# Kernel tuning notes

Measured on AMD Instinct MI355X. Metric: run time of the kernel, lower is better.

Reference implementation:

```python
import jax, jax.numpy as jnp
import numpy as np

B, T, D_IN = 32, 32, 128
N_SLOTS, M_LEN = 512, 64
NUM_SHIFT, NUM_READ, NUM_WRITE = 3, 4, 1
CTRL_DIM = 256
READ_HEAD_LEN = 3 + M_LEN + NUM_SHIFT            # k, beta, g, s, gamma
WRITE_HEAD_LEN = READ_HEAD_LEN + 2 * M_LEN       # + erase, add vectors
INSTR_DIM = NUM_READ * READ_HEAD_LEN + NUM_WRITE * WRITE_HEAD_LEN


def setup_inputs() -> dict:
    key = jax.random.key(0)
    ks = jax.random.split(key, 4)
    def glorot(k, shape):
        lim = np.sqrt(6.0 / (shape[0] + shape[1])).astype(np.float32)
        return jax.random.uniform(k, shape, jnp.float32, -lim, lim)
    return {
        "x": jax.random.normal(ks[0], (B, T, D_IN), jnp.float32),
        "Wc": glorot(ks[1], (D_IN + NUM_READ * M_LEN, CTRL_DIM)),
        "bc": jnp.zeros((CTRL_DIM,), jnp.float32),
        "heads_kernel": glorot(ks[2], (CTRL_DIM, INSTR_DIM)),
        "heads_bias": jnp.zeros((INSTR_DIM,), jnp.float32),
    }


def _parse_heads(h):
    # h: (B, H, 3 + M + S) -> k, beta, g, s, gamma per _get_weight_vector
    k = h[..., :M_LEN]
    b = jnp.exp(h[..., M_LEN])
    g = jax.nn.sigmoid(h[..., M_LEN + 1])
    s = jax.nn.softmax(h[..., M_LEN + 2:M_LEN + 2 + NUM_SHIFT], axis=-1)
    t = jax.nn.softplus(h[..., M_LEN + 2 + NUM_SHIFT]) + 1.0
    return k, b, g, s, t


def _address(Mem, w_prev, k, b, g, s, t):
    # Mem:(B,N,M) k:(B,H,M) w_prev:(B,H,N) b,g,t:(B,H) s:(B,H,S)
    eps = 1e-8
    Mn = jnp.linalg.norm(Mem, axis=-1)                       # (B,N)
    kn = jnp.linalg.norm(k, axis=-1)                         # (B,H)
    sim = jnp.einsum('bhm,bnm->bhn', k, Mem) / (kn[..., None] * Mn[:, None, :] + eps)
    wc = jax.nn.softmax(b[..., None] * sim, axis=-1)         # content
    wg = g[..., None] * wc + (1.0 - g[..., None]) * w_prev   # gate
    half = NUM_SHIFT // 2                                    # circular shift conv
    wsh = sum(s[..., i:i + 1] * jnp.roll(wg, i - half, axis=-1) for i in range(NUM_SHIFT))
    wt = wsh ** t[..., None]                                 # sharpen
    return wt / (jnp.sum(wt, axis=-1, keepdims=True) + eps)


def _ntm_forward(x, Wc, bc, heads_kernel, heads_bias):
    def step(carry, x_t):
        r, rw, ww, Mem = carry
        # dense controller on [x_t, old read vectors]
        ctrl_in = jnp.concatenate([x_t, r.reshape(B, -1)], axis=-1)
        h = jnp.tanh(ctrl_in @ Wc + bc)                      # controller_out == instr
        instr = h @ heads_kernel + heads_bias                # (B, INSTR_DIM)
        rh = instr[:, :NUM_READ * READ_HEAD_LEN].reshape(B, NUM_READ, READ_HEAD_LEN)
        wh = instr[:, NUM_READ * READ_HEAD_LEN:].reshape(B, NUM_WRITE, WRITE_HEAD_LEN)
        rw_n = _address(Mem, rw, *_parse_heads(rh))
        ww_n = _address(Mem, ww, *_parse_heads(wh[..., :READ_HEAD_LEN]))
        e = wh[..., READ_HEAD_LEN:READ_HEAD_LEN + M_LEN]     # raw erase (no sigmoid, as in source)
        a = wh[..., READ_HEAD_LEN + M_LEN:]                  # raw add
        # erase all heads, then add all heads (source loops erase first)
        Mem = Mem * jnp.prod(1.0 - ww_n[..., :, None] * e[..., None, :], axis=1)
        Mem = Mem + jnp.einsum('bwn,bwm->bnm', ww_n, a)
        r_n = jnp.einsum('bnm,brn->brm', Mem, rw_n)          # read
        return (r_n, rw_n, ww_n, Mem), h

    init = (jnp.zeros((B, NUM_READ, M_LEN), jnp.float32),
            jnp.zeros((B, NUM_READ, N_SLOTS), jnp.float32),
            jnp.zeros((B, NUM_WRITE, N_SLOTS), jnp.float32),
            jnp.zeros((B, N_SLOTS, M_LEN), jnp.float32))
    _, outs = jax.lax.scan(step, init, jnp.swapaxes(x, 0, 1))  # time-major
    return outs[-1]  # return_sequences=False -> last controller output (B, CTRL_DIM)


def reference(x, Wc, bc, heads_kernel, heads_bias):
    return _ntm_forward(x, Wc, bc, heads_kernel, heads_bias)
```

## Files before the change

### kernel.cpp

```cpp
#include <hip/hip_runtime.h>
#include <math.h>

#define BB 32
#define TT 32
#define D_INX 128
#define NSLOT 512
#define MLEN 64
#define NREAD 4
#define NHEAD 5
#define CDIM 256
#define IDIM 478
#define RHL 70
#define NT 512

#define XP_SZ   1048576
#define WCT_OFF XP_SZ
#define HKB_OFF (XP_SZ + 262144)

typedef short bf8 __attribute__((ext_vector_type(8)));
typedef float f32x4 __attribute__((ext_vector_type(4)));

struct SMem {
    float mem[NSLOT * MLEN];
    float w4[NSLOT * 4];
    float ww[NSLOT];
    float mn[NSLOT];
    float ctrl[256];
    float h[CDIM];
    float instr[480];
    float k[NHEAD * MLEN];
    float e[MLEN];
    float a[MLEN];
    float u[NHEAD * NSLOT];
};

__device__ __forceinline__ float rlane(float v, int l) {
    return __int_as_float(__builtin_amdgcn_readlane(__float_as_int(v), l));
}

__device__ __forceinline__ void cvt_hi_lo(const float* a, bf8* hi, bf8* lo) {
    union { unsigned u[4]; bf8 v; } H, L;
#pragma unroll
    for (int p = 0; p < 4; ++p) {
        unsigned hu;
        asm("v_cvt_pk_bf16_f32 %0, %1, %2" : "=v"(hu) : "v"(a[2 * p]), "v"(a[2 * p + 1]));
        H.u[p] = hu;
        float h0 = __uint_as_float(hu << 16);
        float h1 = __uint_as_float(hu & 0xffff0000u);
        float l0 = a[2 * p] - h0;
        float l1 = a[2 * p + 1] - h1;
        unsigned lu;
        asm("v_cvt_pk_bf16_f32 %0, %1, %2" : "=v"(lu) : "v"(l0), "v"(l1));
        L.u[p] = lu;
    }
    *hi = H.v; *lo = L.v;
}

__global__ void pack_kernel(const float* __restrict__ Wc, const float* __restrict__ Hk,
                            float* __restrict__ wct, float* __restrict__ hkb)
{
    int idx = blockIdx.x * 256 + threadIdx.x;
    if (idx < 256 * 256) {
        int i = idx >> 8, col = idx & 255;
        wct[((i >> 3) * 256 + col) * 8 + (i & 7)] = Wc[(128 + i) * 256 + col];
    }
    if (idx < 256 * 478) {
        int i = idx / 478, col = idx - i * 478;
        hkb[((i >> 3) * 478 + col) * 8 + (i & 7)] = Hk[i * 478 + col];
    }
}

__global__ __launch_bounds__(256)
void xpart_kernel(const float* __restrict__ x, const float* __restrict__ Wc,
                  const float* __restrict__ bc, float* __restrict__ xp)
{
    __shared__ float xs[D_INX];
    const int bt = blockIdx.x, col = threadIdx.x;
    if (col < D_INX) xs[col] = x[(size_t)bt * D_INX + col];
    __syncthreads();
    float acc = bc[col];
#pragma unroll 8
    for (int k = 0; k < D_INX; ++k) acc += xs[k] * Wc[k * 256 + col];
    xp[(size_t)bt * CDIM + col] = acc;
}

#define P1_CHUNK(cg_) do {                                                      \
    const float4 w0 = wqa[(cg_) * 512];                                         \
    const float4 w1 = wqa[(cg_) * 512 + 1];                                     \
    const int k0 = (cg_) * 8;                                                   \
    float a0 = rlane(creg[(k0 + 0) >> 6], (k0 + 0) & 63);                       \
    float a1 = rlane(creg[(k0 + 1) >> 6], (k0 + 1) & 63);                       \
    float a2 = rlane(creg[(k0 + 2) >> 6], (k0 + 2) & 63);                       \
    float a3 = rlane(creg[(k0 + 3) >> 6], (k0 + 3) & 63);                       \
    float a4 = rlane(creg[(k0 + 4) >> 6], (k0 + 4) & 63);                       \
    float a5 = rlane(creg[(k0 + 5) >> 6], (k0 + 5) & 63);                       \
    float a6 = rlane(creg[(k0 + 6) >> 6], (k0 + 6) & 63);                       \
    float a7 = rlane(creg[(k0 + 7) >> 6], (k0 + 7) & 63);                       \
    accs[(cg_) & 3] += w0.x * a0 + w0.y * a1 + w0.z * a2 + w0.w * a3            \
                     + w1.x * a4 + w1.y * a5 + w1.z * a6 + w1.w * a7;           \
} while (0)

__global__ __launch_bounds__(NT, 2)
void ntm_kernel(const float* __restrict__ xp,
                const float* __restrict__ hb,
                const float* __restrict__ wct,
                const float* __restrict__ hkb,
                float* __restrict__ out)
{
    extern __shared__ float smem_f[];
    SMem* sc = (SMem*)smem_f;

    const int b    = blockIdx.x;
    const int tid  = threadIdx.x;
    const int lane = tid & 63;
    const int wave = tid >> 6;

    const int col   = tid & 255;
    const int halfw = tid >> 8;

    const float hbv = (tid < IDIM) ? hb[tid] : 0.f;

    {
        float4 z4 = make_float4(0.f, 0.f, 0.f, 0.f);
        float4* m4 = (float4*)sc->mem;
        for (int i = tid; i < NSLOT * MLEN / 4; i += NT) m4[i] = z4;
        for (int i = tid; i < NSLOT * 4; i += NT) sc->w4[i] = 0.f;
        if (tid < NSLOT) sc->ww[tid] = 0.f;
        if (tid < 256) sc->ctrl[tid] = 0.f;
    }
    __syncthreads();

    for (int t = 0; t < TT; ++t) {
        {
            const float xpv = xp[(size_t)(b * TT + t) * CDIM + col];

            float creg[4];
            creg[0] = sc->ctrl[lane];
            creg[1] = sc->ctrl[64 + lane];
            creg[2] = sc->ctrl[128 + lane];
            creg[3] = sc->ctrl[192 + lane];

            const float4* wqa = (const float4*)wct + col * 2;
            float accs[4] = {0.f, 0.f, 0.f, 0.f};
            if (halfw == 0) {
#pragma unroll
                for (int cc = 0; cc < 16; ++cc) P1_CHUNK(cc);
            } else {
#pragma unroll
                for (int cc = 0; cc < 16; ++cc) P1_CHUNK(16 + cc);
            }
            float s = (accs[0] + accs[1]) + (accs[2] + accs[3]);
            if (halfw == 1) sc->u[col] = s;
            __syncthreads();
            if (halfw == 0) {
                float z = xpv + s + sc->u[col];
                z = fminf(fmaxf(z, -15.f), 15.f);
                float ex = __expf(2.f * z);
                float hv = (ex - 1.f) / (ex + 1.f);
                sc->h[col] = hv;
                if (t == TT - 1) out[(size_t)b * CDIM + col] = hv;
            }
        }
        if (t == TT - 1) break;
        __syncthreads();

        {
            float hreg[4];
#pragma unroll
            for (int j = 0; j < 4; ++j) hreg[j] = sc->h[64 * j + lane];
            if (tid < IDIM) {
                const float4* wq2a = (const float4*)hkb + tid * 2;
                float accs[4] = {0.f, 0.f, 0.f, 0.f};
#pragma unroll
                for (int c = 0; c < 32; ++c) {
                    const float4 w0 = wq2a[c * 956];
                    const float4 w1 = wq2a[c * 956 + 1];
                    const int k0 = c * 8;
                    float a0 = rlane(hreg[(k0 + 0) >> 6], (k0 + 0) & 63);
                    float a1 = rlane(hreg[(k0 + 1) >> 6], (k0 + 1) & 63);
                    float a2 = rlane(hreg[(k0 + 2) >> 6], (k0 + 2) & 63);
                    float a3 = rlane(hreg[(k0 + 3) >> 6], (k0 + 3) & 63);
                    float a4 = rlane(hreg[(k0 + 4) >> 6], (k0 + 4) & 63);
                    float a5 = rlane(hreg[(k0 + 5) >> 6], (k0 + 5) & 63);
                    float a6 = rlane(hreg[(k0 + 6) >> 6], (k0 + 6) & 63);
                    float a7 = rlane(hreg[(k0 + 7) >> 6], (k0 + 7) & 63);
                    accs[c & 3] += w0.x * a0 + w0.y * a1 + w0.z * a2 + w0.w * a3
                                 + w1.x * a4 + w1.y * a5 + w1.z * a6 + w1.w * a7;
                }
                float acc = hbv + (accs[0] + accs[1]) + (accs[2] + accs[3]);
                sc->instr[tid] = acc;
                if (tid < 350) {
                    int hh = (tid * 937) >> 16;
                    int m = tid - hh * RHL;
                    if (m < MLEN) sc->k[hh * MLEN + m] = acc;
                } else if (tid < 414) {
                    sc->e[tid - 350] = acc;
                } else {
                    sc->a[tid - 414] = acc;
                }
            } else {
                for (int i = tid - IDIM; i < 256; i += NT - IDIM) sc->ctrl[i] = 0.f;
            }
        }
        __syncthreads();

        {
            const int q   = lane >> 4;
            const int r15 = lane & 15;

            bf8 bhi[2], blo[2];
#pragma unroll
            for (int kc = 0; kc < 2; ++kc) {
                float kb[8];
                if (r15 < NHEAD) {
                    const float4* k4 = (const float4*)(sc->k + r15 * MLEN + kc * 32 + q * 8);
                    float4 kv0 = k4[0], kv1 = k4[1];
                    kb[0] = kv0.x; kb[1] = kv0.y; kb[2] = kv0.z; kb[3] = kv0.w;
                    kb[4] = kv1.x; kb[5] = kv1.y; kb[6] = kv1.z; kb[7] = kv1.w;
                } else {
#pragma unroll
                    for (int i = 0; i < 8; ++i) kb[i] = 0.f;
                }
                cvt_hi_lo(kb, &bhi[kc], &blo[kc]);
            }

#pragma unroll
            for (int tt = 0; tt < 4; ++tt) {
                const int tbase = wave * 64 + tt * 16;
                const int n = tbase + r15;
                const int nx = n & 15;
                const float4* m4 = (const float4*)sc->mem + n * 16;
                f32x4 acc = {0.f, 0.f, 0.f, 0.f};
                float nsq = 0.f;
#pragma unroll
                for (int kc = 0; kc < 2; ++kc) {
                    const int j0 = kc * 8 + q * 2;
                    float4 av0 = m4[j0 ^ nx];
                    float4 av1 = m4[(j0 + 1) ^ nx];
                    float aa[8];
                    aa[0] = av0.x; aa[1] = av0.y; aa[2] = av0.z; aa[3] = av0.w;
                    aa[4] = av1.x; aa[5] = av1.y; aa[6] = av1.z; aa[7] = av1.w;
#pragma unroll
                    for (int i = 0; i < 8; ++i) nsq += aa[i] * aa[i];
                    bf8 ahi, alo;
                    cvt_hi_lo(aa, &ahi, &alo);
                    acc = __builtin_amdgcn_mfma_f32_16x16x32_bf16(ahi, bhi[kc], acc, 0, 0, 0);
                    acc = __builtin_amdgcn_mfma_f32_16x16x32_bf16(ahi, blo[kc], acc, 0, 0, 0);
                    acc = __builtin_amdgcn_mfma_f32_16x16x32_bf16(alo, bhi[kc], acc, 0, 0, 0);
                }
                nsq += __shfl_xor(nsq, 16);
                nsq += __shfl_xor(nsq, 32);
                if (q == 0) sc->mn[n] = sqrtf(nsq);
                if (r15 < NHEAD) {
                    float4 st;
                    st.x = acc[0]; st.y = acc[1]; st.z = acc[2]; st.w = acc[3];
                    *(float4*)&sc->u[r15 * NSLOT + tbase + q * 4] = st;
                }
            }
        }
        __syncthreads();

        if (wave < NHEAD) {
            const int h = wave;
            const float* ins = sc->instr + h * RHL;
            float kv = ins[lane];
            float sq = kv * kv;
#pragma unroll
            for (int off = 32; off; off >>= 1) sq += __shfl_xor(sq, off);
            float kn = sqrtf(sq);
            float beta = __expf(ins[64]);
            float g = 1.f / (1.f + __expf(-ins[65]));
            float v0 = ins[66], v1 = ins[67], v2 = ins[68];
            float mx3 = fmaxf(v0, fmaxf(v1, v2));
            float e0 = __expf(v0 - mx3), e1 = __expf(v1 - mx3), e2 = __expf(v2 - mx3);
            float inv3 = 1.f / (e0 + e1 + e2);
            float s0 = e0 * inv3, s1 = e1 * inv3, s2 = e2 * inv3;
            float tv = ins[69];
            float tp = fmaxf(tv, 0.f) + log1pf(__expf(-fabsf(tv))) + 1.f;

            float uu[8];
#pragma unroll
            for (int j = 0; j < 8; ++j) {
                int slot = j * 64 + lane;
                float d = sc->u[h * NSLOT + slot];
                uu[j] = beta * d / (kn * sc->mn[slot] + 1e-8f);
            }
            float m = uu[0];
#pragma unroll
            for (int j = 1; j < 8; ++j) m = fmaxf(m, uu[j]);
#pragma unroll
            for (int off = 32; off; off >>= 1) m = fmaxf(m, __shfl_xor(m, off));
            float ev[8]; float Z = 0.f;
#pragma unroll
            for (int j = 0; j < 8; ++j) { ev[j] = __expf(uu[j] - m); Z += ev[j]; }
#pragma unroll
            for (int off = 32; off; off >>= 1) Z += __shfl_xor(Z, off);
            float invZ = 1.f / Z;
            float wg[8];
#pragma unroll
            for (int j = 0; j < 8; ++j) {
                int slot = j * 64 + lane;
                float oldw = (h < 4) ? sc->w4[slot * 4 + h] : sc->ww[slot];
                wg[j] = g * ev[j] * invZ + (1.f - g) * oldw;
            }
            int lm = (lane + 63) & 63, lp = (lane + 1) & 63;
            float rm[8], rp[8];
#pragma unroll
            for (int j = 0; j < 8; ++j) {
                float sm = (lane == 63) ? wg[(j + 7) & 7] : wg[j];
                float sp = (lane == 0)  ? wg[(j + 1) & 7] : wg[j];
                rm[j] = __shfl(sm, lm);
                rp[j] = __shfl(sp, lp);
            }
            float wt[8]; float S = 0.f;
#pragma unroll
            for (int j = 0; j < 8; ++j) {
                float wsh = s0 * rp[j] + s1 * wg[j] + s2 * rm[j];
                wt[j] = __builtin_amdgcn_exp2f(tp * __builtin_amdgcn_logf(wsh));
                S += wt[j];
            }
#pragma unroll
            for (int off = 32; off; off >>= 1) S += __shfl_xor(S, off);
            float invS = 1.f / (S + 1e-8f);
#pragma unroll
            for (int j = 0; j < 8; ++j) {
                int slot = j * 64 + lane;
                float wnew = wt[j] * invS;
                if (h < 4) sc->w4[slot * 4 + h] = wnew;
                else       sc->ww[slot] = wnew;
            }
        }
        __syncthreads();

        {
            const int rg = lane >> 4, j = lane & 15, base = wave * 64;
            const float4 ev = ((const float4*)sc->e)[j];
            const float4 av = ((const float4*)sc->a)[j];
            float4* m4 = (float4*)sc->mem;
            float4 ac[4];
#pragma unroll
            for (int hh = 0; hh < 4; ++hh) ac[hh] = make_float4(0.f, 0.f, 0.f, 0.f);
#pragma unroll
            for (int i = 0; i < 16; ++i) {
                const int n = base + 4 * i + rg;
                const int idx = n * 16 + (j ^ (n & 15));
                float4 mv = m4[idx];
                const float wv = sc->ww[n];
                mv.x = mv.x * (1.f - wv * ev.x) + wv * av.x;
                mv.y = mv.y * (1.f - wv * ev.y) + wv * av.y;
                mv.z = mv.z * (1.f - wv * ev.z) + wv * av.z;
                mv.w = mv.w * (1.f - wv * ev.w) + wv * av.w;
                m4[idx] = mv;
                const float4 w4v = ((const float4*)sc->w4)[n];
                ac[0].x += w4v.x * mv.x; ac[0].y += w4v.x * mv.y; ac[0].z += w4v.x * mv.z; ac[0].w += w4v.x * mv.w;
                ac[1].x += w4v.y * mv.x; ac[1].y += w4v.y * mv.y; ac[1].z += w4v.y * mv.z; ac[1].w += w4v.y * mv.w;
                ac[2].x += w4v.z * mv.x; ac[2].y += w4v.z * mv.y; ac[2].z += w4v.z * mv.z; ac[2].w += w4v.z * mv.w;
                ac[3].x += w4v.w * mv.x; ac[3].y += w4v.w * mv.y; ac[3].z += w4v.w * mv.z; ac[3].w += w4v.w * mv.w;
            }
            float* af = (float*)ac;
#pragma unroll
            for (int q = 0; q < 16; ++q) {
                af[q] += __shfl_xor(af[q], 16);
                af[q] += __shfl_xor(af[q], 32);
            }
            if (rg == 0) {
#pragma unroll
                for (int hh = 0; hh < 4; ++hh) {
                    atomicAdd(&sc->ctrl[hh * 64 + 4 * j + 0], ac[hh].x);
                    atomicAdd(&sc->ctrl[hh * 64 + 4 * j + 1], ac[hh].y);
                    atomicAdd(&sc->ctrl[hh * 64 + 4 * j + 2], ac[hh].z);
                    atomicAdd(&sc->ctrl[hh * 64 + 4 * j + 3], ac[hh].w);
                }
            }
        }
        __syncthreads();
    }
}

extern "C" void kernel_launch(void* const* d_in, const int* in_sizes, int n_in,
                              void* d_out, int out_size, void* d_ws, size_t ws_size,
                              hipStream_t stream) {
    const float* x  = (const float*)d_in[0];
    const float* Wc = (const float*)d_in[1];
    const float* bc = (const float*)d_in[2];
    const float* Hk = (const float*)d_in[3];
    const float* hb = (const float*)d_in[4];
    float* out = (float*)d_out;

    float* xp  = (float*)d_ws;
    float* wct = (float*)((char*)d_ws + WCT_OFF);
    float* hkb = (float*)((char*)d_ws + HKB_OFF);

    static_assert(sizeof(SMem) <= 163840, "LDS overflow");
    (void)hipFuncSetAttribute((const void*)ntm_kernel,
                              hipFuncAttributeMaxDynamicSharedMemorySize,
                              (int)sizeof(SMem));

    hipLaunchKernelGGL(pack_kernel, dim3(478), dim3(256), 0, stream, Wc, Hk, wct, hkb);
    hipLaunchKernelGGL(xpart_kernel, dim3(BB * TT), dim3(256), 0, stream, x, Wc, bc, xp);
    hipLaunchKernelGGL(ntm_kernel, dim3(BB), dim3(NT), sizeof(SMem), stream,
                       xp, hb, wct, hkb, out);
}
```

Before: 744.5 us.

## Compute memory read via split-bf16 MFMA and per-wave partials instead of atomics

Replaces the scalar FMA read accumulation plus shuffles and LDS atomicAdds with bf16 hi/lo split MFMA products of read weights against the updated memory tile. Each wave writes its partial read vectors to a new per-wave buffer, and these are summed into ctrl at the start of the next step. This aims to cut FP ALU work and atomic contention. In exchange it adds gather-style LDS loads for the MFMA operands, an extra barrier per step, and the approximation error of the three-term bf16 split.

```diff
diff --git a/kernel.cpp b/kernel.cpp
--- a/kernel.cpp
+++ b/kernel.cpp
@@ -127,10 +127,19 @@
         for (int i = tid; i < NSLOT * 4; i += NT) sc->w4[i] = 0.f;
         if (tid < NSLOT) sc->ww[tid] = 0.f;
         if (tid < 256) sc->ctrl[tid] = 0.f;
+        for (int i = tid; i < 2048; i += NT) sc->u[i] = 0.f;
     }
     __syncthreads();
 
     for (int t = 0; t < TT; ++t) {
+        if (tid < 256) {
+            float s = sc->u[tid];
+#pragma unroll
+            for (int w = 1; w < 8; ++w) s += sc->u[w * 256 + tid];
+            sc->ctrl[tid] = s;
+        }
+        __syncthreads();
+
         {
             const float xpv = xp[(size_t)(b * TT + t) * CDIM + col];
 
@@ -198,8 +207,6 @@
                 } else {
                     sc->a[tid - 414] = acc;
                 }
-            } else {
-                for (int i = tid - IDIM; i < 256; i += NT - IDIM) sc->ctrl[i] = 0.f;
             }
         }
         __syncthreads();
@@ -225,8 +232,8 @@
             }
 
 #pragma unroll
-            for (int tt = 0; tt < 4; ++tt) {
-                const int tbase = wave * 64 + tt * 16;
+            for (int tt2 = 0; tt2 < 4; ++tt2) {
+                const int tbase = wave * 64 + tt2 * 16;
                 const int n = tbase + r15;
                 const int nx = n & 15;
                 const float4* m4 = (const float4*)sc->mem + n * 16;
@@ -337,9 +344,6 @@
             const float4 ev = ((const float4*)sc->e)[j];
             const float4 av = ((const float4*)sc->a)[j];
             float4* m4 = (float4*)sc->mem;
-            float4 ac[4];
-#pragma unroll
-            for (int hh = 0; hh < 4; ++hh) ac[hh] = make_float4(0.f, 0.f, 0.f, 0.f);
 #pragma unroll
             for (int i = 0; i < 16; ++i) {
                 const int n = base + 4 * i + rg;
@@ -351,25 +355,41 @@
                 mv.z = mv.z * (1.f - wv * ev.z) + wv * av.z;
                 mv.w = mv.w * (1.f - wv * ev.w) + wv * av.w;
                 m4[idx] = mv;
-                const float4 w4v = ((const float4*)sc->w4)[n];
-                ac[0].x += w4v.x * mv.x; ac[0].y += w4v.x * mv.y; ac[0].z += w4v.x * mv.z; ac[0].w += w4v.x * mv.w;
-                ac[1].x += w4v.y * mv.x; ac[1].y += w4v.y * mv.y; ac[1].z += w4v.y * mv.z; ac[1].w += w4v.y * mv.w;
-                ac[2].x += w4v.z * mv.x; ac[2].y += w4v.z * mv.y; ac[2].z += w4v.z * mv.z; ac[2].w += w4v.z * mv.w;
-                ac[3].x += w4v.w * mv.x; ac[3].y += w4v.w * mv.y; ac[3].z += w4v.w * mv.z; ac[3].w += w4v.w * mv.w;
-            }
-            float* af = (float*)ac;
-#pragma unroll
-            for (int q = 0; q < 16; ++q) {
-                af[q] += __shfl_xor(af[q], 16);
-                af[q] += __shfl_xor(af[q], 32);
-            }
-            if (rg == 0) {
-#pragma unroll
-                for (int hh = 0; hh < 4; ++hh) {
-                    atomicAdd(&sc->ctrl[hh * 64 + 4 * j + 0], ac[hh].x);
-                    atomicAdd(&sc->ctrl[hh * 64 + 4 * j + 1], ac[hh].y);
-                    atomicAdd(&sc->ctrl[hh * 64 + 4 * j + 2], ac[hh].z);
-                    atomicAdd(&sc->ctrl[hh * 64 + 4 * j + 3], ac[hh].w);
+            }
+            const int q = rg, r15 = j;
+            bf8 ahi[2], alo[2];
+#pragma unroll
+            for (int kc = 0; kc < 2; ++kc) {
+                float ab[8];
+#pragma unroll
+                for (int i = 0; i < 8; ++i) {
+                    const int n2 = base + kc * 32 + q * 8 + i;
+                    ab[i] = (r15 < 4) ? sc->w4[n2 * 4 + r15] : 0.f;
+                }
+                cvt_hi_lo(ab, &ahi[kc], &alo[kc]);
+            }
+#pragma unroll
+            for (int tt2 = 0; tt2 < 4; ++tt2) {
+                f32x4 acc = {0.f, 0.f, 0.f, 0.f};
+#pragma unroll
+                for (int kc = 0; kc < 2; ++kc) {
+                    float bb[8];
+#pragma unroll
+                    for (int i = 0; i < 8; ++i) {
+                        const int n2 = base + kc * 32 + q * 8 + i;
+                        const int cc = tt2 * 16 + r15;
+                        bb[i] = sc->mem[n2 * 64 + (((cc >> 2) ^ (n2 & 15)) << 2) + (cc & 3)];
+                    }
+                    bf8 bhi, blo;
+                    cvt_hi_lo(bb, &bhi, &blo);
+                    acc = __builtin_amdgcn_mfma_f32_16x16x32_bf16(ahi[kc], bhi, acc, 0, 0, 0);
+                    acc = __builtin_amdgcn_mfma_f32_16x16x32_bf16(ahi[kc], blo, acc, 0, 0, 0);
+                    acc = __builtin_amdgcn_mfma_f32_16x16x32_bf16(alo[kc], bhi, acc, 0, 0, 0);
+                }
+                if (q == 0) {
+#pragma unroll
+                    for (int reg = 0; reg < 4; ++reg)
+                        sc->u[wave * 256 + reg * 64 + tt2 * 16 + r15] = acc[reg];
                 }
             }
         }
```

After: 742.7 us, median of 3. About the same (-0.2%).
